# Performance work log

Measured on AMD Instinct MI355X. Metric: run time of the kernel, lower is better.

The kernel has to match this reference:

```python
import jax, jax.numpy as jnp
import numpy as np

G, N, E = 4, 50000, 800000
F_IN, HID, OUT = 64, 128, 64


def setup_inputs() -> dict:
    key = jax.random.key(0)
    ks = jax.random.split(key, 4)
    x = jax.random.normal(ks[0], (G, N, F_IN), dtype=jnp.float32)
    edge_index = jax.random.randint(ks[1], (G, 2, E), 0, N)
    W1 = jax.random.normal(ks[2], (G, F_IN, HID), dtype=jnp.float32) / np.sqrt(F_IN).astype(np.float32)
    b1 = jnp.zeros((G, HID), dtype=jnp.float32)
    W2 = jax.random.normal(ks[3], (G, HID, OUT), dtype=jnp.float32) / np.sqrt(HID).astype(np.float32)
    b2 = jnp.zeros((G, OUT), dtype=jnp.float32)
    return {"x": x, "edge_index": edge_index, "W1": W1, "b1": b1, "W2": W2, "b2": b2}


def gcn_conv(x, src, dst, W, b):
    # PyG GCNConv: add self loops, symmetric norm D^-1/2 (A+I) D^-1/2, then XW + b
    n = x.shape[0]
    loop = jnp.arange(n)
    s = jnp.concatenate([src, loop])  # [E+N]
    d = jnp.concatenate([dst, loop])
    deg = jax.ops.segment_sum(jnp.ones_like(s, dtype=x.dtype), d, num_segments=n)
    dinv = jax.lax.rsqrt(deg)  # deg >= 1 because of self loops
    norm = dinv[s] * dinv[d]  # [E+N]
    h = x @ W  # [N, F_out]
    msg = h[s] * norm[:, None]  # edge-wise gather (memory-bound)
    out = jax.ops.segment_sum(msg, d, num_segments=n)  # scatter-add
    return out + b


def reference(x, edge_index, W1, b1, W2, b2):
    def per_graph(xg, eg, w1, b1g, w2, b2g):
        src, dst = eg[0], eg[1]
        h = jax.nn.elu(gcn_conv(xg, src, dst, w1, b1g))
        h = jax.nn.elu(gcn_conv(h, src, dst, w2, b2g))
        return h  # [N, OUT]

    out = jax.vmap(per_graph)(x, edge_index, W1, b1, W2, b2)  # [G, N, OUT]
    return out.reshape(G * N, OUT)  # torch.cat over graphs along dim 0
```

## Files before the change

kernel.cpp:

```cpp
#include <hip/hip_runtime.h>
#include <cstdint>

constexpr int G = 4, N = 50000, E = 800000;
constexpr int FIN = 64, HID = 128, FOUT = 64;
constexpr int NB = (N + 1023) / 1024;

constexpr int PB = 64;
constexpr int CP = E / PB;
constexpr int NBK = (N + 255) / 256;

typedef unsigned short ushort;
typedef _Float16 f16;

__device__ __forceinline__ ushort f2h(float f) {
  f16 h = (f16)f;
  return __builtin_bit_cast(ushort, h);
}
__device__ __forceinline__ float h2f(ushort u) {
  f16 h = __builtin_bit_cast(f16, u);
  return (float)h;
}

__device__ __forceinline__ void xcd_map(int b, int& g, int& chunk) {
  int xcd = b & 7;
  int sub = b >> 3;
  g = xcd >> 1;
  chunk = (xcd & 1) * 6250 + sub;
}

__global__ void k_x2h(const float4* __restrict__ X, const float* __restrict__ dinv,
                      ushort4* __restrict__ Xh, int n4) {
  int i = blockIdx.x * blockDim.x + threadIdx.x;
  if (i >= n4) return;
  float sc = dinv[i >> 4];
  float4 v = X[i];
  ushort4 o = {f2h(sc * v.x), f2h(sc * v.y), f2h(sc * v.z), f2h(sc * v.w)};
  Xh[i] = o;
}


__global__ __launch_bounds__(256) void k_phist(const int* __restrict__ ei,
                                               int* __restrict__ PH) {
  __shared__ int h[NBK];
  int pb = blockIdx.x, g = blockIdx.y;
  for (int i = threadIdx.x; i < NBK; i += 256) h[i] = 0;
  __syncthreads();
  const int4* dst4 = (const int4*)(ei + (size_t)g * 2 * E + E + (size_t)pb * CP);
  for (int i = threadIdx.x; i < CP / 4; i += 256) {
    int4 d = dst4[i];
    atomicAdd(&h[d.x >> 8], 1);
    atomicAdd(&h[d.y >> 8], 1);
    atomicAdd(&h[d.z >> 8], 1);
    atomicAdd(&h[d.w >> 8], 1);
  }
  __syncthreads();
  for (int i = threadIdx.x; i < NBK; i += 256)
    PH[((size_t)g * NBK + i) * PB + pb] = h[i];
}

__global__ void k_pscan(const int* __restrict__ PH, int* __restrict__ POFF,
                        int* __restrict__ BB) {
  int g = blockIdx.x, k = threadIdx.x;
  int tot = 0;
  if (k < NBK) {
#pragma unroll 8
    for (int pb = 0; pb < PB; ++pb) tot += PH[((size_t)g * NBK + k) * PB + pb];
  }
  __shared__ int sm[256];
  sm[k] = tot;
  __syncthreads();
  for (int off = 1; off < 256; off <<= 1) {
    int v = (k >= off) ? sm[k - off] : 0;
    __syncthreads();
    sm[k] += v;
    __syncthreads();
  }
  int excl = sm[k] - tot;
  if (k < NBK) {
    BB[g * (NBK + 1) + k] = excl;
    if (k == NBK - 1) BB[g * (NBK + 1) + NBK] = excl + tot;
    int run = excl;
#pragma unroll 8
    for (int pb = 0; pb < PB; ++pb) {
      POFF[((size_t)g * NBK + k) * PB + pb] = run;
      run += PH[((size_t)g * NBK + k) * PB + pb];
    }
  }
}

__global__ __launch_bounds__(256) void k_part(const int* __restrict__ ei,
                                              const int* __restrict__ POFF,
                                              unsigned* __restrict__ pairs) {
  __shared__ int off[NBK];
  __shared__ int rk[NBK];
  int pb = blockIdx.x, g = blockIdx.y;
  for (int i = threadIdx.x; i < NBK; i += 256) {
    off[i] = POFF[((size_t)g * NBK + i) * PB + pb];
    rk[i] = 0;
  }
  __syncthreads();
  const int* base = ei + (size_t)g * 2 * E + (size_t)pb * CP;
  const int4* s4 = (const int4*)base;
  const int4* d4 = (const int4*)(base + E);
  unsigned* pg = pairs + (size_t)g * E;
  for (int i = threadIdx.x; i < CP / 4; i += 256) {
    int4 s = s4[i], d = d4[i];
    int sv[4] = {s.x, s.y, s.z, s.w};
    int dv[4] = {d.x, d.y, d.z, d.w};
#pragma unroll
    for (int k = 0; k < 4; ++k) {
      int b = dv[k] >> 8;
      int r = atomicAdd(&rk[b], 1);
      pg[off[b] + r] = (unsigned)sv[k] | ((unsigned)(dv[k] & 255) << 16);
    }
  }
}

__global__ __launch_bounds__(256) void k_bcnt(const unsigned* __restrict__ pairs,
                                              const int* __restrict__ BB,
                                              int* __restrict__ cnt) {
  __shared__ int h[256];
  int k = blockIdx.x, g = blockIdx.y;
  h[threadIdx.x] = 0;
  __syncthreads();
  int lo = BB[g * (NBK + 1) + k], hi = BB[g * (NBK + 1) + k + 1];
  const unsigned* pg = pairs + (size_t)g * E;
  for (int i = lo + (int)threadIdx.x; i < hi; i += 256)
    atomicAdd(&h[(pg[i] >> 16) & 255], 1);
  __syncthreads();
  int n0 = k << 8;
  int nn = min(256, N - n0);
  if ((int)threadIdx.x < nn) cnt[g * N + n0 + threadIdx.x] = h[threadIdx.x];
}

__global__ __launch_bounds__(256) void k_place(const unsigned* __restrict__ pairs,
                                               const int* __restrict__ BB,
                                               const int* __restrict__ rowptr,
                                               int* __restrict__ col) {
  __shared__ int rp[256];
  __shared__ int rk[256];
  int k = blockIdx.x, g = blockIdx.y;
  int n0 = k << 8;
  int nn = min(256, N - n0);
  if ((int)threadIdx.x < nn) rp[threadIdx.x] = rowptr[g * (N + 1) + n0 + threadIdx.x];
  rk[threadIdx.x] = 0;
  __syncthreads();
  int lo = BB[g * (NBK + 1) + k], hi = BB[g * (NBK + 1) + k + 1];
  const unsigned* pg = pairs + (size_t)g * E;
  int* cg = col + (size_t)g * E;
  for (int i = lo + (int)threadIdx.x; i < hi; i += 256) {
    unsigned p = pg[i];
    int dl = (p >> 16) & 255;
    int r = atomicAdd(&rk[dl], 1);
    cg[rp[dl] + r] = (int)(p & 0xffffu);
  }
}

__global__ void k_scan_partial(const int* __restrict__ cnt, int* __restrict__ part) {
  int g = blockIdx.y, b = blockIdx.x, tid = threadIdx.x;
  int base = b * 1024 + tid * 4;
  int s = 0;
#pragma unroll
  for (int k = 0; k < 4; ++k) {
    int i = base + k;
    if (i < N) s += cnt[g * N + i];
  }
  __shared__ int sm[256];
  sm[tid] = s;
  __syncthreads();
  for (int off = 128; off > 0; off >>= 1) {
    if (tid < off) sm[tid] += sm[tid + off];
    __syncthreads();
  }
  if (tid == 0) part[g * NB + b] = sm[0];
}

__global__ void k_scan_mid(int* __restrict__ part, int* __restrict__ rowptr) {
  int g = blockIdx.x;
  if (threadIdx.x != 0) return;
  int run = 0;
  for (int b = 0; b < NB; ++b) {
    int t = part[g * NB + b];
    part[g * NB + b] = run;
    run += t;
  }
  rowptr[g * (N + 1) + N] = run;
}

__global__ void k_scan_final(const int* __restrict__ cnt, const int* __restrict__ part,
                             int* __restrict__ rowptr, float* __restrict__ dinv) {
  int g = blockIdx.y, b = blockIdx.x, tid = threadIdx.x;
  int base = b * 1024 + tid * 4;
  int c[4];
  int s = 0;
#pragma unroll
  for (int k = 0; k < 4; ++k) {
    int i = base + k;
    c[k] = (i < N) ? cnt[g * N + i] : 0;
    s += c[k];
  }
  __shared__ int sm[256];
  sm[tid] = s;
  __syncthreads();
  for (int off = 1; off < 256; off <<= 1) {
    int v = (tid >= off) ? sm[tid - off] : 0;
    __syncthreads();
    sm[tid] += v;
    __syncthreads();
  }
  int excl = sm[tid] - s + part[g * NB + b];
#pragma unroll
  for (int k = 0; k < 4; ++k) {
    int i = base + k;
    if (i < N) {
      rowptr[g * (N + 1) + i] = excl;
      dinv[g * N + i] = rsqrtf((float)(c[k] + 1));
    }
    excl += c[k];
  }
}

template <int K, int F, bool PRESCALE, bool BIASELU, bool OUTH>
__global__ __launch_bounds__(256) void k_gemm_lds(const float* __restrict__ X,
                                                  const float* __restrict__ W,
                                                  const float* __restrict__ dinv,
                                                  const float* __restrict__ bias,
                                                  void* __restrict__ Hout) {
  constexpr int CH = F / 4;
  constexpr int PK = K + 1;
  __shared__ float xs[64 * PK];
  int g = blockIdx.y;
  int R0 = blockIdx.x * 64;
  for (int idx = threadIdx.x; idx < 64 * K; idx += 256) {
    int r = idx / K, k = idx - r * K;
    int row = R0 + r;
    xs[r * PK + k] = (row < N) ? X[((size_t)g * N + row) * K + k] : 0.f;
  }
  __syncthreads();
  int wv = threadIdx.x >> 6;
  int lane = threadIdx.x & 63;
  int c0 = __builtin_amdgcn_readfirstlane(wv * CH);
  const float* Wg = W + (size_t)g * K * F;
  const float* xrow = &xs[lane * PK];
  float acc[CH];
#pragma unroll
  for (int c = 0; c < CH; ++c) acc[c] = 0.f;
#pragma unroll 4
  for (int k = 0; k < K; ++k) {
    float xv = xrow[k];
#pragma unroll
    for (int c = 0; c < CH; ++c)
      acc[c] = fmaf(xv, Wg[(size_t)k * F + c0 + c], acc[c]);
  }
  int row = R0 + lane;
  if (row >= N) return;
  if constexpr (PRESCALE) {
    float sc = dinv[g * N + row];
#pragma unroll
    for (int c = 0; c < CH; ++c) acc[c] *= sc;
  }
  if constexpr (BIASELU) {
#pragma unroll
    for (int c = 0; c < CH; ++c) {
      float v = acc[c] + bias[g * F + c0 + c];
      acc[c] = v > 0.f ? v : expm1f(v);
    }
  }
  if constexpr (OUTH) {
    ushort* opb = (ushort*)Hout + ((size_t)g * N + row) * F + c0;
#pragma unroll
    for (int c4 = 0; c4 < CH; c4 += 4) {
      ushort4 o = {f2h(acc[c4]), f2h(acc[c4 + 1]), f2h(acc[c4 + 2]),
                   f2h(acc[c4 + 3])};
      *(ushort4*)(opb + c4) = o;
    }
  } else {
    float* op = (float*)Hout + ((size_t)g * N + row) * F + c0;
#pragma unroll
    for (int c4 = 0; c4 < CH; c4 += 4) {
      float4 o = {acc[c4], acc[c4 + 1], acc[c4 + 2], acc[c4 + 3]};
      *(float4*)(op + c4) = o;
    }
  }
}

__device__ __forceinline__ float agg_row(const ushort* __restrict__ hb,
                                         const int* __restrict__ cl, int rs, int re,
                                         int lane, float acc) {
  int j = rs;
  for (; j + 16 <= re; j += 16) {
    int s[16];
#pragma unroll
    for (int k = 0; k < 16; ++k) s[k] = cl[j + k];
    float v[16];
#pragma unroll
    for (int k = 0; k < 16; ++k) v[k] = h2f(hb[(size_t)s[k] * 64 + lane]);
#pragma unroll
    for (int k = 0; k < 16; ++k) acc += v[k];
  }
  for (; j + 8 <= re; j += 8) {
    int s[8];
#pragma unroll
    for (int k = 0; k < 8; ++k) s[k] = cl[j + k];
    float v[8];
#pragma unroll
    for (int k = 0; k < 8; ++k) v[k] = h2f(hb[(size_t)s[k] * 64 + lane]);
#pragma unroll
    for (int k = 0; k < 8; ++k) acc += v[k];
  }
  for (; j < re; ++j) acc += h2f(hb[(size_t)cl[j] * 64 + lane]);
  return acc;
}

template <int F>
__global__ __launch_bounds__(256) void k_agg_in(const ushort* __restrict__ Xh,
                                                const int* __restrict__ rowptr,
                                                const int* __restrict__ col,
                                                const float* __restrict__ dinv,
                                                float* __restrict__ Z) {
  int g, chunk;
  xcd_map(blockIdx.x, g, chunk);
  int d = __builtin_amdgcn_readfirstlane(chunk * 4 + (threadIdx.x >> 6));
  int lane = threadIdx.x & 63;
  const ushort* hb = Xh + (size_t)g * N * F;
  const int* cl = col + (size_t)g * E;
  int rs = rowptr[g * (N + 1) + d];
  int re = rowptr[g * (N + 1) + d + 1];
  float acc = h2f(hb[(size_t)d * F + lane]);
  acc = agg_row(hb, cl, rs, re, lane, acc);
  Z[((size_t)g * N + d) * F + lane] = dinv[g * N + d] * acc;
}

template <int F>
__global__ __launch_bounds__(256) void k_agg_out(const ushort* __restrict__ Hsrc,
                                                 const int* __restrict__ rowptr,
                                                 const int* __restrict__ col,
                                                 const float* __restrict__ dinv,
                                                 const float* __restrict__ bias,
                                                 float* __restrict__ out) {
  int g, chunk;
  xcd_map(blockIdx.x, g, chunk);
  int d = __builtin_amdgcn_readfirstlane(chunk * 4 + (threadIdx.x >> 6));
  int lane = threadIdx.x & 63;
  const ushort* hb = Hsrc + (size_t)g * N * F;
  const int* cl = col + (size_t)g * E;
  int rs = rowptr[g * (N + 1) + d];
  int re = rowptr[g * (N + 1) + d + 1];
  float acc = h2f(hb[(size_t)d * F + lane]);
  acc = agg_row(hb, cl, rs, re, lane, acc);
  float p = acc * dinv[g * N + d] + bias[g * F + lane];
  p = p > 0.f ? p : expm1f(p);
  out[((size_t)g * N + d) * F + lane] = p;
}

extern "C" void kernel_launch(void* const* d_in, const int* in_sizes, int n_in,
                              void* d_out, int out_size, void* d_ws, size_t ws_size,
                              hipStream_t stream) {
  const float* x = (const float*)d_in[0];
  const int* ei = (const int*)d_in[1];
  const float* W1 = (const float*)d_in[2];
  const float* b1 = (const float*)d_in[3];
  const float* W2 = (const float*)d_in[4];
  const float* b2 = (const float*)d_in[5];
  float* out = (float*)d_out;

  char* p = (char*)d_ws;
  auto alloc = [&](size_t bytes) {
    char* r = p;
    p += (bytes + 255) & ~(size_t)255;
    return r;
  };
  int* cnt = (int*)alloc(sizeof(int) * G * N);
  int* rowptr = (int*)alloc(sizeof(int) * G * (N + 1));
  int* part = (int*)alloc(sizeof(int) * G * NB);
  float* dinv = (float*)alloc(sizeof(float) * G * N);
  int* col = (int*)alloc(sizeof(int) * (size_t)G * E);
  float* z = (float*)alloc(sizeof(float) * (size_t)G * N * FIN);
  float* h1 = (float*)alloc(sizeof(float) * (size_t)G * N * HID);
  ushort* h2s = (ushort*)z;
  unsigned* pairs = (unsigned*)h1;
  int* PH = (int*)((char*)h1 + ((size_t)13 << 20));
  int* POFF = (int*)((char*)h1 + ((size_t)14 << 20));
  int* BB = (int*)((char*)h1 + ((size_t)15 << 20));
  ushort* xh = (ushort*)((char*)h1 + ((size_t)32 << 20));

  k_phist<<<dim3(PB, G), 256, 0, stream>>>(ei, PH);
  k_pscan<<<G, 256, 0, stream>>>(PH, POFF, BB);
  k_part<<<dim3(PB, G), 256, 0, stream>>>(ei, POFF, pairs);
  k_bcnt<<<dim3(NBK, G), 256, 0, stream>>>(pairs, BB, cnt);
  dim3 sg(NB, G);
  k_scan_partial<<<sg, 256, 0, stream>>>(cnt, part);
  k_scan_mid<<<G, 64, 0, stream>>>(part, rowptr);
  k_scan_final<<<sg, 256, 0, stream>>>(cnt, part, rowptr, dinv);
  k_place<<<dim3(NBK, G), 256, 0, stream>>>(pairs, BB, rowptr, col);

  k_x2h<<<(G * N * FIN / 4 + 255) / 256, 256, 0, stream>>>(
      (const float4*)x, dinv, (ushort4*)xh, G * N * FIN / 4);

  k_agg_in<FIN><<<(G * N) / 4, 256, 0, stream>>>(xh, rowptr, col, dinv, z);
  dim3 gg((N + 63) / 64, G);
  k_gemm_lds<FIN, HID, false, true, false>
      <<<gg, 256, 0, stream>>>(z, W1, nullptr, b1, h1);

  k_gemm_lds<HID, FOUT, true, false, true>
      <<<gg, 256, 0, stream>>>(h1, W2, dinv, nullptr, h2s);
  k_agg_out<FOUT><<<(G * N) / 4, 256, 0, stream>>>(h2s, rowptr, col, dinv, b2, out);
}
```

Measured before the change: 516.8 us.

## Fuse two dense GEMMs into one MLP kernel keeping hidden layer on-chip

```diff
diff --git a/kernel.cpp b/kernel.cpp
--- a/kernel.cpp
+++ b/kernel.cpp
@@ -220,15 +220,16 @@
   }
 }
 
-template <int K, int F, bool PRESCALE, bool BIASELU, bool OUTH>
-__global__ __launch_bounds__(256) void k_gemm_lds(const float* __restrict__ X,
-                                                  const float* __restrict__ W,
-                                                  const float* __restrict__ dinv,
-                                                  const float* __restrict__ bias,
-                                                  void* __restrict__ Hout) {
-  constexpr int CH = F / 4;
+__global__ __launch_bounds__(256) void k_mlp(const float* __restrict__ X,
+                                             const float* __restrict__ W1,
+                                             const float* __restrict__ b1,
+                                             const float* __restrict__ W2,
+                                             const float* __restrict__ dinv,
+                                             ushort* __restrict__ H2s) {
+  constexpr int K = FIN;
   constexpr int PK = K + 1;
-  __shared__ float xs[64 * PK];
+  __shared__ float lds[4 * 32 * 65];
+  float* xs = lds;
   int g = blockIdx.y;
   int R0 = blockIdx.x * 64;
   for (int idx = threadIdx.x; idx < 64 * K; idx += 256) {
@@ -239,47 +240,68 @@
   __syncthreads();
   int wv = threadIdx.x >> 6;
   int lane = threadIdx.x & 63;
-  int c0 = __builtin_amdgcn_readfirstlane(wv * CH);
-  const float* Wg = W + (size_t)g * K * F;
+  int c0 = __builtin_amdgcn_readfirstlane(wv * 32);
+  const float* W1g = W1 + (size_t)g * K * HID;
   const float* xrow = &xs[lane * PK];
-  float acc[CH];
-#pragma unroll
-  for (int c = 0; c < CH; ++c) acc[c] = 0.f;
+  float acc[32];
+#pragma unroll
+  for (int c = 0; c < 32; ++c) acc[c] = 0.f;
 #pragma unroll 4
   for (int k = 0; k < K; ++k) {
     float xv = xrow[k];
 #pragma unroll
-    for (int c = 0; c < CH; ++c)
-      acc[c] = fmaf(xv, Wg[(size_t)k * F + c0 + c], acc[c]);
-  }
-  int row = R0 + lane;
-  if (row >= N) return;
-  if constexpr (PRESCALE) {
-    float sc = dinv[g * N + row];
-#pragma unroll
-    for (int c = 0; c < CH; ++c) acc[c] *= sc;
-  }
-  if constexpr (BIASELU) {
-#pragma unroll
-    for (int c = 0; c < CH; ++c) {
-      float v = acc[c] + bias[g * F + c0 + c];
-      acc[c] = v > 0.f ? v : expm1f(v);
+    for (int c = 0; c < 32; ++c)
+      acc[c] = fmaf(xv, W1g[(size_t)k * HID + c0 + c], acc[c]);
+  }
+#pragma unroll
+  for (int c = 0; c < 32; ++c) {
+    float v = acc[c] + b1[g * HID + c0 + c];
+    acc[c] = v > 0.f ? v : expm1f(v);
+  }
+  const float* W2g = W2 + (size_t)g * HID * FOUT;
+  int rrow = threadIdx.x >> 2;
+  int jg = threadIdx.x & 3;
+  for (int h = 0; h < 2; ++h) {
+    float ph[32];
+#pragma unroll
+    for (int j = 0; j < 32; ++j) ph[j] = 0.f;
+    for (int c = 0; c < 32; ++c) {
+      const float* wr = &W2g[(size_t)(c0 + c) * FOUT + h * 32];
+      float av = acc[c];
+#pragma unroll
+      for (int j = 0; j < 32; ++j) ph[j] = fmaf(av, wr[j], ph[j]);
     }
-  }
-  if constexpr (OUTH) {
-    ushort* opb = (ushort*)Hout + ((size_t)g * N + row) * F + c0;
-#pragma unroll
-    for (int c4 = 0; c4 < CH; c4 += 4) {
-      ushort4 o = {f2h(acc[c4]), f2h(acc[c4 + 1]), f2h(acc[c4 + 2]),
-                   f2h(acc[c4 + 3])};
-      *(ushort4*)(opb + c4) = o;
-    }
-  } else {
-    float* op = (float*)Hout + ((size_t)g * N + row) * F + c0;
-#pragma unroll
-    for (int c4 = 0; c4 < CH; c4 += 4) {
-      float4 o = {acc[c4], acc[c4 + 1], acc[c4 + 2], acc[c4 + 3]};
-      *(float4*)(op + c4) = o;
+    __syncthreads();
+#pragma unroll
+    for (int j = 0; j < 32; ++j) lds[wv * 2080 + j * 65 + lane] = ph[j];
+    __syncthreads();
+    if (R0 + rrow < N) {
+      float dd = dinv[g * N + R0 + rrow];
+      ushort4 oa, ob;
+      {
+        int j = jg * 8;
+        float s0 = lds[j * 65 + rrow] + lds[2080 + j * 65 + rrow] +
+                   lds[4160 + j * 65 + rrow] + lds[6240 + j * 65 + rrow];
+        float s1 = lds[(j + 1) * 65 + rrow] + lds[2080 + (j + 1) * 65 + rrow] +
+                   lds[4160 + (j + 1) * 65 + rrow] + lds[6240 + (j + 1) * 65 + rrow];
+        float s2 = lds[(j + 2) * 65 + rrow] + lds[2080 + (j + 2) * 65 + rrow] +
+                   lds[4160 + (j + 2) * 65 + rrow] + lds[6240 + (j + 2) * 65 + rrow];
+        float s3 = lds[(j + 3) * 65 + rrow] + lds[2080 + (j + 3) * 65 + rrow] +
+                   lds[4160 + (j + 3) * 65 + rrow] + lds[6240 + (j + 3) * 65 + rrow];
+        oa = {f2h(s0 * dd), f2h(s1 * dd), f2h(s2 * dd), f2h(s3 * dd)};
+        float s4 = lds[(j + 4) * 65 + rrow] + lds[2080 + (j + 4) * 65 + rrow] +
+                   lds[4160 + (j + 4) * 65 + rrow] + lds[6240 + (j + 4) * 65 + rrow];
+        float s5 = lds[(j + 5) * 65 + rrow] + lds[2080 + (j + 5) * 65 + rrow] +
+                   lds[4160 + (j + 5) * 65 + rrow] + lds[6240 + (j + 5) * 65 + rrow];
+        float s6 = lds[(j + 6) * 65 + rrow] + lds[2080 + (j + 6) * 65 + rrow] +
+                   lds[4160 + (j + 6) * 65 + rrow] + lds[6240 + (j + 6) * 65 + rrow];
+        float s7 = lds[(j + 7) * 65 + rrow] + lds[2080 + (j + 7) * 65 + rrow] +
+                   lds[4160 + (j + 7) * 65 + rrow] + lds[6240 + (j + 7) * 65 + rrow];
+        ob = {f2h(s4 * dd), f2h(s5 * dd), f2h(s6 * dd), f2h(s7 * dd)};
+      }
+      ushort* dst = H2s + ((size_t)g * N + R0 + rrow) * FOUT + h * 32 + jg * 8;
+      *(ushort4*)dst = oa;
+      *(ushort4*)(dst + 4) = ob;
     }
   }
 }
@@ -376,13 +398,13 @@
   float* dinv = (float*)alloc(sizeof(float) * G * N);
   int* col = (int*)alloc(sizeof(int) * (size_t)G * E);
   float* z = (float*)alloc(sizeof(float) * (size_t)G * N * FIN);
-  float* h1 = (float*)alloc(sizeof(float) * (size_t)G * N * HID);
+  char* scratch = (char*)alloc((size_t)103 << 20);
   ushort* h2s = (ushort*)z;
-  unsigned* pairs = (unsigned*)h1;
-  int* PH = (int*)((char*)h1 + ((size_t)13 << 20));
-  int* POFF = (int*)((char*)h1 + ((size_t)14 << 20));
-  int* BB = (int*)((char*)h1 + ((size_t)15 << 20));
-  ushort* xh = (ushort*)((char*)h1 + ((size_t)32 << 20));
+  unsigned* pairs = (unsigned*)scratch;
+  int* PH = (int*)(scratch + ((size_t)13 << 20));
+  int* POFF = (int*)(scratch + ((size_t)14 << 20));
+  int* BB = (int*)(scratch + ((size_t)15 << 20));
+  ushort* xh = (ushort*)(scratch + ((size_t)32 << 20));
 
   k_phist<<<dim3(PB, G), 256, 0, stream>>>(ei, PH);
   k_pscan<<<G, 256, 0, stream>>>(PH, POFF, BB);
@@ -398,11 +420,9 @@
       (const float4*)x, dinv, (ushort4*)xh, G * N * FIN / 4);
 
   k_agg_in<FIN><<<(G * N) / 4, 256, 0, stream>>>(xh, rowptr, col, dinv, z);
+
   dim3 gg((N + 63) / 64, G);
-  k_gemm_lds<FIN, HID, false, true, false>
-      <<<gg, 256, 0, stream>>>(z, W1, nullptr, b1, h1);
-
-  k_gemm_lds<HID, FOUT, true, false, true>
-      <<<gg, 256, 0, stream>>>(h1, W2, dinv, nullptr, h2s);
+  k_mlp<<<gg, 256, 0, stream>>>(z, W1, b1, W2, dinv, h2s);
+
   k_agg_out<FOUT><<<(G * N) / 4, 256, 0, stream>>>(h2s, rowptr, col, dinv, b2, out);
 }
```

Result: faster. 483.5 us (-6.5%).
